# Performance work log

Measured on AMD Instinct MI355X. Metric: run time of the kernel, lower is better.

Reference implementation:

```python
import jax, jax.numpy as jnp
import numpy as np

EPS = 1e-8
UNTANH = 0.5                       # hp UNTANH (blend factor, assumed)
BUNTANH_SCALE = (2.0 + 2.0 ** 0.5) ** 0.5  # sqrt(2 + sqrt(2)) from source
C_MOMENT = 0.99                    # hp c_moment
A_VARIANCE = 0.02                  # hp a_variance
SINKHORN_ITERS = 8


def rms_norm(x, axes):
    ms = jnp.mean(x * x, axis=axes, keepdims=True)
    return x * jax.lax.rsqrt(ms + EPS)


def buntanh(x):
    # blended un-tanh: untanh * identity + (1-untanh) * tanh, rescaled
    return BUNTANH_SCALE * (UNTANH * x + (1.0 - UNTANH) * jnp.tanh(x))


def sinkhorn_knopp(A, n_iter=SINKHORN_ITERS):
    A = jnp.maximum(A, 0.0) + EPS
    def body(A, _):
        A = A / jnp.sum(A, axis=-1, keepdims=True)  # row normalize
        A = A / jnp.sum(A, axis=-2, keepdims=True)  # col normalize
        return A, None
    A, _ = jax.lax.scan(body, A, None, length=n_iter)
    return A


def setup_inputs() -> dict:
    key = jax.random.key(0)
    ks = jax.random.split(key, 8)
    B, N, D, IN_DIM = 4, 1024, 128, 8192
    inv_sqrt_d = 1.0 / np.sqrt(D)
    return {
        "state": jax.random.normal(ks[0], (B, N, D), jnp.float32) * 0.1,
        "output": jax.random.normal(ks[1], (B, N, D), jnp.float32) * 0.1,
        "w1": jax.random.normal(ks[2], (B, N, D, D), jnp.float32) * inv_sqrt_d,
        "w2": jax.random.normal(ks[3], (B, N, D, D), jnp.float32) * inv_sqrt_d,
        "w3": jax.random.normal(ks[4], (B, N, D, D), jnp.float32) * inv_sqrt_d,
        "A_ema": jax.random.normal(ks[5], (B, N, N), jnp.float32) * 0.01,
        "env_input": jax.random.normal(ks[6], (B, IN_DIM), jnp.float32),
        "noise": jax.random.normal(ks[7], (B, N, D), jnp.float32),
    }


def reference(state, output, w1, w2, w3, A_ema, env_input, noise):
    B, N, D = state.shape
    input_dim = env_input.shape[1]
    num_in = -(-input_dim // D)  # ceil

    # first-call mask/EMA adjustment (num_input_nodes change branch)
    A_mask = jnp.ones((N, N), dtype=state.dtype).at[:num_in, :].set(0.0)
    A_ema = A_ema.at[:, num_in, :num_in].add(3.0 / num_in)

    # per-node batched small GEMMs + custom activation
    Q = buntanh(jnp.einsum('bnd,bndk->bnk', state, w3))
    K = buntanh(jnp.einsum('bnd,bndk->bnk', state, w2))
    prediction = buntanh(jnp.einsum('bnd,bndk->bnk', state, w1))

    # QK^T adjacency, rms-normed over full [N,N]
    raw_A = jnp.einsum('bnk,bmk->bnm', Q, K) / jnp.sqrt(jnp.asarray(D, state.dtype))
    raw_A = rms_norm(raw_A, (-2, -1))

    # EMA (non-first step) + input-node masking
    new_A_ema = (A_ema * C_MOMENT + raw_A * (1.0 - C_MOMENT)) * A_mask

    # doubly-stochastic projection, thresholded sparsification, re-project
    dsA = sinkhorn_knopp(new_A_ema)
    baseline = 1.0 / (N + 1.0)
    sparse_A = jnp.where(dsA > baseline, dsA, 0.0)
    A = sinkhorn_knopp(sparse_A) * A_mask

    # boredom noise scaled by variance deficit (torch var is unbiased)
    var = jnp.var(A, axis=(-2, -1), keepdims=True, ddof=1)
    vd = jax.nn.relu(A_VARIANCE - var)
    V = output + vd * noise

    # message passing + softsign, overwrite input-node rows with env input
    target = jax.nn.soft_sign(jnp.einsum('bnm,bmd->bnd', A, V))
    pad = num_in * D - input_dim
    env = jnp.pad(env_input, ((0, 0), (0, pad))).reshape(B, num_in, D)
    target = target.at[:, :num_in, :].set(env)

    out = jnp.concatenate([target, prediction], axis=-1)  # [B,N,2D]
    return out, A
```

## Files before the change

kernel.cpp:

```cpp
#include <hip/hip_runtime.h>
#include <math.h>

#define NB 4
#define NN 1024
#define ND 128
#define NUM_IN 64
#define F_EPS 1e-8f
#define BT_SCALE 1.8477590650225735f
#define INV_SQRT_D 0.08838834764831844f
#define BASELINE (1.0f/1025.0f)
#define OUT_STRIDE 256
#define A_OFF 1048576

__device__ __forceinline__ float buntanh_f(float x) {
    return BT_SCALE * (0.5f * x + 0.5f * tanhf(x));
}
__device__ __forceinline__ float wave_sum(float v) {
    #pragma unroll
    for (int off = 32; off > 0; off >>= 1) v += __shfl_xor(v, off, 64);
    return v;
}
__device__ __forceinline__ float bflo(unsigned u) { return __uint_as_float(u << 16); }
__device__ __forceinline__ float bfhi(unsigned u) { return __uint_as_float(u & 0xffff0000u); }
__device__ __forceinline__ unsigned bf_rne(float f) {
    unsigned x = __float_as_uint(f);
    return (x + 0x7fffu + ((x >> 16) & 1u)) >> 16;
}
__device__ __forceinline__ unsigned bf_pack(float lo, float hi) {
    return bf_rne(lo) | (bf_rne(hi) << 16);
}

typedef float f32x4 __attribute__((ext_vector_type(4)));
__device__ __forceinline__ float4 ntload4(const float4* p) {
    f32x4 v = __builtin_nontemporal_load((const f32x4*)p);
    return make_float4(v.x, v.y, v.z, v.w);
}

__global__ __launch_bounds__(256, 6) void qkp_kernel(
    const float* __restrict__ state,
    const float* __restrict__ w1,
    const float* __restrict__ w2,
    const float* __restrict__ w3,
    float* __restrict__ dout,
    float* __restrict__ Qg,
    float* __restrict__ Kg)
{
    const int blk = blockIdx.x;
    const int node = ((blk & 7) << 9) | (blk >> 3);

    __shared__ float s_state[ND];
    __shared__ float4 red[3][8][32];

    const int t = threadIdx.x;
    if (t < 32) ((float4*)s_state)[t] =
        ((const float4*)(state + ((size_t)node << 7)))[t];
    __syncthreads();

    const int g = t >> 5, m = t & 31;

    auto do_mat = [&](const float* wbase, int q) {
        const float4* w4 = (const float4*)(wbase + ((size_t)node << 14));
        float4 wv[8];
        float4 acc = make_float4(0.f, 0.f, 0.f, 0.f);
        #pragma unroll
        for (int i = 0; i < 8; ++i) wv[i] = ntload4(&w4[i*256 + t]);
        #pragma unroll
        for (int i = 0; i < 8; ++i) {
            const float s = s_state[i*8 + g];
            acc.x += s*wv[i].x; acc.y += s*wv[i].y;
            acc.z += s*wv[i].z; acc.w += s*wv[i].w;
        }
        #pragma unroll
        for (int i = 0; i < 8; ++i) wv[i] = ntload4(&w4[(8+i)*256 + t]);
        #pragma unroll
        for (int i = 0; i < 8; ++i) {
            const float s = s_state[(8+i)*8 + g];
            acc.x += s*wv[i].x; acc.y += s*wv[i].y;
            acc.z += s*wv[i].z; acc.w += s*wv[i].w;
        }
        red[q][g][m] = acc;
    };
    do_mat(w1, 0);
    do_mat(w2, 1);
    do_mat(w3, 2);
    __syncthreads();

    if (t < 96) {
        const int q = t >> 5, mm = t & 31;
        float4 o = red[q][0][mm];
        #pragma unroll
        for (int gg = 1; gg < 8; ++gg) {
            const float4 r = red[q][gg][mm];
            o.x += r.x; o.y += r.y; o.z += r.z; o.w += r.w;
        }
        o.x = buntanh_f(o.x); o.y = buntanh_f(o.y);
        o.z = buntanh_f(o.z); o.w = buntanh_f(o.w);
        if (q == 0) {
            *(float4*)(dout + (size_t)node * OUT_STRIDE + ND + 4*mm) = o;
        } else {
            float* base = (q == 1) ? Kg : Qg;
            *(float4*)(base + ((size_t)node << 7) + 4*mm) = o;
        }
    }
}

__global__ __launch_bounds__(256) void qk2_kernel(
    const float* __restrict__ Qg, const float* __restrict__ Kg,
    unsigned* __restrict__ rawbf, float* __restrict__ reds)
{
    const int b = blockIdx.x >> 10;
    const int tile = blockIdx.x & 1023;
    const int tr = tile >> 5, tc = tile & 31;

    __shared__ float Qs[32][132];
    __shared__ float Ks[32][136];
    __shared__ float wr4[4];

    const int t = threadIdx.x;
    for (int i = t; i < 1024; i += 256) {
        const int r = i >> 5, q = i & 31;
        *(float4*)&Qs[r][q*4] = *(const float4*)(Qg + (((size_t)(b*NN + tr*32 + r)) << 7) + q*4);
        *(float4*)&Ks[r][q*4] = *(const float4*)(Kg + (((size_t)(b*NN + tc*32 + r)) << 7) + q*4);
    }
    __syncthreads();

    const int ty = t >> 4;
    const int tx = t & 15;
    float a00=0.f, a01=0.f, a10=0.f, a11=0.f;
    #pragma unroll
    for (int dq = 0; dq < 32; ++dq) {
        const float4 q0 = *(const float4*)&Qs[ty][dq*4];
        const float4 q1 = *(const float4*)&Qs[ty+16][dq*4];
        const float4 k0 = *(const float4*)&Ks[2*tx][dq*4];
        const float4 k1 = *(const float4*)&Ks[2*tx+1][dq*4];
        a00 += q0.x*k0.x + q0.y*k0.y + q0.z*k0.z + q0.w*k0.w;
        a01 += q0.x*k1.x + q0.y*k1.y + q0.z*k1.z + q0.w*k1.w;
        a10 += q1.x*k0.x + q1.y*k0.y + q1.z*k0.z + q1.w*k0.w;
        a11 += q1.x*k1.x + q1.y*k1.y + q1.z*k1.z + q1.w*k1.w;
    }
    a00 *= INV_SQRT_D; a01 *= INV_SQRT_D; a10 *= INV_SQRT_D; a11 *= INV_SQRT_D;

    unsigned* r0p = rawbf + (((size_t)(b*NN + tr*32 + ty)) << 9) + tc*16;
    unsigned* r1p = rawbf + (((size_t)(b*NN + tr*32 + ty + 16)) << 9) + tc*16;
    r0p[tx] = bf_pack(a00, a01);
    r1p[tx] = bf_pack(a10, a11);

    float ssq = a00*a00 + a01*a01 + a10*a10 + a11*a11;
    ssq = wave_sum(ssq);
    if ((t & 63) == 0) wr4[t >> 6] = ssq;
    __syncthreads();
    if (t == 0) atomicAdd(&reds[b], wr4[0]+wr4[1]+wr4[2]+wr4[3]);
}

__global__ __launch_bounds__(256) void emaT_kernel(
    const unsigned* __restrict__ rawbf, const float* __restrict__ A_ema,
    const float* __restrict__ reds,
    unsigned* __restrict__ M0, unsigned* __restrict__ M0T,
    float* __restrict__ SR)
{
    const int b = blockIdx.x >> 8;
    const int tile = blockIdx.x & 255;
    const int tr = tile >> 4, tc = tile & 15;
    const int R0 = tr << 6, C0 = tc << 6;

    __shared__ float st[64][65];
    __shared__ float s_part[64][5];

    const int t = threadIdx.x;
    const int r = t >> 2, q = t & 3;
    const int row = R0 + r;
    const float scale = rsqrtf(reds[b] * (1.0f/1048576.0f) + F_EPS);

    const unsigned* rawrow = rawbf + (((size_t)(b*NN + row)) << 9) + tc*8*4;
    const uint4 u0 = ((const uint4*)rawrow)[q*2];
    const uint4 u1 = ((const uint4*)rawrow)[q*2 + 1];
    float rv[16];
    rv[0]=bflo(u0.x); rv[1]=bfhi(u0.x); rv[2]=bflo(u0.y); rv[3]=bfhi(u0.y);
    rv[4]=bflo(u0.z); rv[5]=bfhi(u0.z); rv[6]=bflo(u0.w); rv[7]=bfhi(u0.w);
    rv[8]=bflo(u1.x); rv[9]=bfhi(u1.x); rv[10]=bflo(u1.y); rv[11]=bfhi(u1.y);
    rv[12]=bflo(u1.z); rv[13]=bfhi(u1.z); rv[14]=bflo(u1.w); rv[15]=bfhi(u1.w);

    const float* emarow = A_ema + (((size_t)(b*NN + row)) << 10) + C0 + q*16;
    float s = 0.f;
    #pragma unroll
    for (int j = 0; j < 4; ++j) {
        const float4 e = ((const float4*)emarow)[j];
        float ev[4] = {e.x, e.y, e.z, e.w};
        #pragma unroll
        for (int k = 0; k < 4; ++k) {
            const int e_idx = j*4 + k;
            const int c = C0 + q*16 + e_idx;
            float em = ev[k];
            if (row == NUM_IN && c < NUM_IN) em += 3.0f / NUM_IN;
            float v = em * 0.99f + rv[e_idx] * scale * 0.01f;
            if (row < NUM_IN) v = 0.f;
            v = fmaxf(v, 0.f) + F_EPS;
            rv[e_idx] = v;
            st[r][q*16 + e_idx] = v;
            s += v;
        }
    }
    s_part[r][q] = s;

    unsigned* m0row = M0 + (((size_t)(b*NN + row)) << 9) + tc*8*4;
    uint4 o0, o1;
    o0.x = bf_pack(rv[0],rv[1]);  o0.y = bf_pack(rv[2],rv[3]);
    o0.z = bf_pack(rv[4],rv[5]);  o0.w = bf_pack(rv[6],rv[7]);
    o1.x = bf_pack(rv[8],rv[9]);  o1.y = bf_pack(rv[10],rv[11]);
    o1.z = bf_pack(rv[12],rv[13]); o1.w = bf_pack(rv[14],rv[15]);
    ((uint4*)m0row)[q*2]     = o0;
    ((uint4*)m0row)[q*2 + 1] = o1;
    __syncthreads();

    if (t < 64) {
        const float rs = s_part[t][0] + s_part[t][1] + s_part[t][2] + s_part[t][3];
        atomicAdd(&SR[b*NN + R0 + t], rs);
    }

    const int cT = t >> 2;
    float tv[16];
    #pragma unroll
    for (int k = 0; k < 16; ++k) tv[k] = st[q*16 + k][cT];
    uint4 w0, w1;
    w0.x = bf_pack(tv[0],tv[1]);  w0.y = bf_pack(tv[2],tv[3]);
    w0.z = bf_pack(tv[4],tv[5]);  w0.w = bf_pack(tv[6],tv[7]);
    w1.x = bf_pack(tv[8],tv[9]);  w1.y = bf_pack(tv[10],tv[11]);
    w1.z = bf_pack(tv[12],tv[13]); w1.w = bf_pack(tv[14],tv[15]);
    unsigned* mtrow = M0T + (((size_t)(b*NN + C0 + cT)) << 9) + tr*8*4;
    ((uint4*)mtrow)[q*2]     = w0;
    ((uint4*)mtrow)[q*2 + 1] = w1;
}

template<bool INV_IN>
__global__ __launch_bounds__(256) void mv_kernel(
    const unsigned* __restrict__ Abf, const float* __restrict__ x,
    float* __restrict__ y)
{
    const int blk = blockIdx.x;
    const int lp  = ((blk & 7) << 5) | (blk >> 3);
    const int b   = lp >> 6;
    const int r0  = (lp & 63) << 4;
    const int t = threadIdx.x;
    const int w = t >> 6, l = t & 63;

    const float4* xb = (const float4*)(x + (b << 10));
    float4 x0 = xb[2*l], x1 = xb[2*l+1], x2 = xb[128+2*l], x3 = xb[129+2*l];
    if (INV_IN) {
        x0.x=1.f/x0.x; x0.y=1.f/x0.y; x0.z=1.f/x0.z; x0.w=1.f/x0.w;
        x1.x=1.f/x1.x; x1.y=1.f/x1.y; x1.z=1.f/x1.z; x1.w=1.f/x1.w;
        x2.x=1.f/x2.x; x2.y=1.f/x2.y; x2.z=1.f/x2.z; x2.w=1.f/x2.w;
        x3.x=1.f/x3.x; x3.y=1.f/x3.y; x3.z=1.f/x3.z; x3.w=1.f/x3.w;
    }

    #pragma unroll
    for (int r = 0; r < 4; ++r) {
        const int row = r0 + (w << 2) + r;
        const unsigned* rp = Abf + (((size_t)((b << 10) + row)) << 9);
        const uint4 v0 = ((const uint4*)rp)[l];
        const uint4 v1 = ((const uint4*)rp)[64 + l];
        float a = bflo(v0.x)*x0.x + bfhi(v0.x)*x0.y
                + bflo(v0.y)*x0.z + bfhi(v0.y)*x0.w
                + bflo(v0.z)*x1.x + bfhi(v0.z)*x1.y
                + bflo(v0.w)*x1.z + bfhi(v0.w)*x1.w
                + bflo(v1.x)*x2.x + bfhi(v1.x)*x2.y
                + bflo(v1.y)*x2.z + bfhi(v1.y)*x2.w
                + bflo(v1.z)*x3.x + bfhi(v1.z)*x3.y
                + bflo(v1.w)*x3.z + bfhi(v1.w)*x3.w;
        a = wave_sum(a);
        if (l == 0) y[(b << 10) + row] = 1.0f / a;
    }
}

__global__ __launch_bounds__(256) void thresh_kernel(
    const unsigned* __restrict__ M0, const unsigned* __restrict__ M0T,
    const float* __restrict__ r8, const float* __restrict__ c8,
    unsigned* __restrict__ A1, unsigned* __restrict__ A1T,
    float* __restrict__ SR2)
{
    const int t = threadIdx.x;
    const int b = blockIdx.x >> 6;
    const int g0 = (blockIdx.x & 63) << 4;
    const int w = t >> 6, l = t & 63;
    const bool doA1 = (w < 2);
    const int wr = doA1 ? w : (w - 2);
    const unsigned* src = doA1 ? M0 : M0T;
    unsigned*       dst = doA1 ? A1 : A1T;
    const float* rowS = doA1 ? r8 : c8;
    const float* colS = doA1 ? c8 : r8;

    const float4* cb = (const float4*)(colS + (b << 10));
    const float4 c0 = cb[2*l], c1 = cb[2*l+1], c2 = cb[128+2*l], c3 = cb[129+2*l];
    const float cm[16] = {c0.x,c0.y,c0.z,c0.w, c1.x,c1.y,c1.z,c1.w,
                          c2.x,c2.y,c2.z,c2.w, c3.x,c3.y,c3.z,c3.w};

    for (int rr = 0; rr < 8; ++rr) {
        const int row = g0 + wr*8 + rr;
        const float ri = rowS[(b << 10) + row];
        const unsigned* rp = src + (((size_t)(b*NN + row)) << 9);
        const uint4 v0 = ((const uint4*)rp)[l];
        const uint4 v1 = ((const uint4*)rp)[64 + l];
        float e[16];
        e[0]=bflo(v0.x); e[1]=bfhi(v0.x); e[2]=bflo(v0.y); e[3]=bfhi(v0.y);
        e[4]=bflo(v0.z); e[5]=bfhi(v0.z); e[6]=bflo(v0.w); e[7]=bfhi(v0.w);
        e[8]=bflo(v1.x); e[9]=bfhi(v1.x); e[10]=bflo(v1.y); e[11]=bfhi(v1.y);
        e[12]=bflo(v1.z); e[13]=bfhi(v1.z); e[14]=bflo(v1.w); e[15]=bfhi(v1.w);
        float s = 0.f;
        #pragma unroll
        for (int j = 0; j < 16; ++j) {
            const float d = e[j] * ri * cm[j];
            e[j] = (d > BASELINE ? d : 0.f) + F_EPS;
            s += e[j];
        }
        uint4 o0, o1;
        o0.x = bf_pack(e[0],e[1]);  o0.y = bf_pack(e[2],e[3]);
        o0.z = bf_pack(e[4],e[5]);  o0.w = bf_pack(e[6],e[7]);
        o1.x = bf_pack(e[8],e[9]);  o1.y = bf_pack(e[10],e[11]);
        o1.z = bf_pack(e[12],e[13]); o1.w = bf_pack(e[14],e[15]);
        unsigned* op = dst + (((size_t)(b*NN + row)) << 9);
        ((uint4*)op)[l] = o0;
        ((uint4*)op)[64 + l] = o1;
        if (doA1) {
            s = wave_sum(s);
            if (l == 0) SR2[b*NN + row] = s;
        }
    }
}

__global__ __launch_bounds__(256) void fin_kernel(
    const unsigned* __restrict__ A1, const float* __restrict__ r8,
    const float* __restrict__ c8, float* __restrict__ reds,
    float* __restrict__ dout)
{
    __shared__ float wred[8];
    const int t = threadIdx.x;
    const int b = blockIdx.x >> 6;
    const int g0 = (blockIdx.x & 63) << 4;
    const int w = t >> 6, l = t & 63;

    const float4* cb = (const float4*)(c8 + (b << 10));
    const float4 c0 = cb[2*l], c1 = cb[2*l+1], c2 = cb[128+2*l], c3 = cb[129+2*l];
    const float cm[16] = {c0.x,c0.y,c0.z,c0.w, c1.x,c1.y,c1.z,c1.w,
                          c2.x,c2.y,c2.z,c2.w, c3.x,c3.y,c3.z,c3.w};

    float s1 = 0.f, s2 = 0.f;
    for (int rr = 0; rr < 4; ++rr) {
        const int row = g0 + w*4 + rr;
        float* Arow = dout + A_OFF + (((size_t)(b*NN + row)) << 10);
        if (row < NUM_IN) {
            const float4 z = make_float4(0.f,0.f,0.f,0.f);
            ((float4*)Arow)[2*l] = z;       ((float4*)Arow)[2*l+1] = z;
            ((float4*)Arow)[128+2*l] = z;   ((float4*)Arow)[129+2*l] = z;
        } else {
            const float ri = r8[(b << 10) + row];
            const unsigned* rp = A1 + (((size_t)(b*NN + row)) << 9);
            const uint4 v0 = ((const uint4*)rp)[l];
            const uint4 v1 = ((const uint4*)rp)[64 + l];
            float e[16];
            e[0]=bflo(v0.x); e[1]=bfhi(v0.x); e[2]=bflo(v0.y); e[3]=bfhi(v0.y);
            e[4]=bflo(v0.z); e[5]=bfhi(v0.z); e[6]=bflo(v0.w); e[7]=bfhi(v0.w);
            e[8]=bflo(v1.x); e[9]=bfhi(v1.x); e[10]=bflo(v1.y); e[11]=bfhi(v1.y);
            e[12]=bflo(v1.z); e[13]=bfhi(v1.z); e[14]=bflo(v1.w); e[15]=bfhi(v1.w);
            #pragma unroll
            for (int j = 0; j < 16; ++j) {
                e[j] = e[j] * ri * cm[j];
                s1 += e[j]; s2 += e[j]*e[j];
            }
            ((float4*)Arow)[2*l]     = make_float4(e[0],e[1],e[2],e[3]);
            ((float4*)Arow)[2*l+1]   = make_float4(e[4],e[5],e[6],e[7]);
            ((float4*)Arow)[128+2*l] = make_float4(e[8],e[9],e[10],e[11]);
            ((float4*)Arow)[129+2*l] = make_float4(e[12],e[13],e[14],e[15]);
        }
    }
    s1 = wave_sum(s1); s2 = wave_sum(s2);
    if (l == 0) { wred[w] = s1; wred[4 + w] = s2; }
    __syncthreads();
    if (t == 0) {
        atomicAdd(&reds[4 + b], wred[0]+wred[1]+wred[2]+wred[3]);
        atomicAdd(&reds[8 + b], wred[4]+wred[5]+wred[6]+wred[7]);
    }
}

__global__ __launch_bounds__(256) void vbuild_kernel(
    const float* __restrict__ outp, const float* __restrict__ noise,
    const float* __restrict__ reds, float* __restrict__ V)
{
    const int i = blockIdx.x * 256 + threadIdx.x;
    const int b = i >> 15;
    const float Mn = 1048576.f;
    const float S1 = reds[4 + b], S2 = reds[8 + b];
    const float var = (S2 - S1*S1/Mn) / (Mn - 1.f);
    const float vd = fmaxf(0.02f - var, 0.f);
    const float4 o = ((const float4*)outp)[i];
    const float4 n = ((const float4*)noise)[i];
    ((float4*)V)[i] = make_float4(o.x + vd*n.x, o.y + vd*n.y,
                                  o.z + vd*n.z, o.w + vd*n.w);
}

__global__ __launch_bounds__(256) void av_part(
    const float* __restrict__ A,
    const float* __restrict__ V,
    float* __restrict__ P)
{
    const int bid = blockIdx.x;
    const int ks = bid & 3;
    const int rt = (bid >> 2) % 60;
    const int b  = bid / 240;
    const int r0 = NUM_IN + rt * 16;
    const int mc0 = ks << 8;
    const int t = threadIdx.x;
    const int d = t & 127, rg = t >> 7;
    const int rowb = r0 + rg*8;

    float acc[8] = {0.f,0.f,0.f,0.f,0.f,0.f,0.f,0.f};
    const float* Vb = V + ((size_t)b << 17) + ((size_t)mc0 << 7) + d;
    const float* Ab = A + (((size_t)(b*NN + rowb)) << 10) + mc0;

    #pragma unroll 4
    for (int mq = 0; mq < 64; ++mq) {
        const float v0 = Vb[(mq*4 + 0) << 7];
        const float v1 = Vb[(mq*4 + 1) << 7];
        const float v2 = Vb[(mq*4 + 2) << 7];
        const float v3 = Vb[(mq*4 + 3) << 7];
        #pragma unroll
        for (int k = 0; k < 8; ++k) {
            const float4 a = *(const float4*)(Ab + ((size_t)k << 10) + mq*4);
            acc[k] += a.x*v0 + a.y*v1 + a.z*v2 + a.w*v3;
        }
    }
    #pragma unroll
    for (int k = 0; k < 8; ++k) {
        const int ridx = rt*16 + rg*8 + k;
        P[(((size_t)(ks*NB + b)) * 960 + ridx) * 128 + d] = acc[k];
    }
}

__global__ __launch_bounds__(256) void av_fin(
    const float* __restrict__ P, const float* __restrict__ env,
    float* __restrict__ dout)
{
    const int t = threadIdx.x;
    int bid = blockIdx.x;
    if (bid < 128) {
        const int idx = bid*256 + t;
        const int b = idx >> 13, off = idx & 8191;
        const int r = off >> 7, d = off & 127;
        dout[((size_t)(b*NN + r)) * OUT_STRIDE + d] = env[idx];
        return;
    }
    bid -= 128;
    const int idx = bid*256 + t;
    const int d = idx & 127;
    const int rd = idx >> 7;
    const int b = rd / 960;
    const int ridx = rd - b*960;
    const float s = P[idx] + P[idx + 491520] + P[idx + 2*491520] + P[idx + 3*491520];
    dout[((size_t)(b*NN + NUM_IN + ridx)) * OUT_STRIDE + d] = s / (1.f + fabsf(s));
}

extern "C" void kernel_launch(void* const* d_in, const int* in_sizes, int n_in,
                              void* d_out, int out_size, void* d_ws, size_t ws_size,
                              hipStream_t stream)
{
    (void)in_sizes; (void)n_in; (void)out_size; (void)ws_size;
    const float* state = (const float*)d_in[0];
    const float* outp  = (const float*)d_in[1];
    const float* w1    = (const float*)d_in[2];
    const float* w2    = (const float*)d_in[3];
    const float* w3    = (const float*)d_in[4];
    const float* A_ema = (const float*)d_in[5];
    const float* env   = (const float*)d_in[6];
    const float* noise = (const float*)d_in[7];
    float* dout = (float*)d_out;

    unsigned* M0  = (unsigned*)(dout + A_OFF);
    unsigned* M0T = M0 + 2097152;

    float*    Qg   = (float*)d_ws;
    float*    Kg   = Qg + 524288;
    float*    Vg   = Kg + 524288;
    unsigned* raw  = (unsigned*)(Vg + 524288);
    unsigned* A1   = raw;
    unsigned* A1T  = raw + 2097152;
    float*    Pp   = (float*)A1T;
    float*    SR1  = (float*)(A1T + 2097152);
    float*    reds = SR1 + 4096;
    float*    SC1  = reds + 16;
    float*    SR2  = SC1 + 4096;
    float*    SC2  = SR2 + 4096;
    float*    RV1  = SC2 + 4096;
    float*    RV2  = RV1 + 4096;

    hipMemsetAsync(SR1, 0, (4096 + 16) * sizeof(float), stream);

    qkp_kernel<<<dim3(NB*NN), dim3(256), 0, stream>>>(
        state, w1, w2, w3, dout, Qg, Kg);

    qk2_kernel<<<dim3(NB*1024), dim3(256), 0, stream>>>(Qg, Kg, raw, reds);

    emaT_kernel<<<dim3(NB*256), dim3(256), 0, stream>>>(
        raw, A_ema, reds, M0, M0T, SR1);

    mv_kernel<true ><<<dim3(256), dim3(256), 0, stream>>>(M0T, SR1, SC1);
    for (int k = 1; k < 15; ++k) {
        if (k & 1)
            mv_kernel<false><<<dim3(256), dim3(256), 0, stream>>>(M0, SC1, RV1);
        else
            mv_kernel<false><<<dim3(256), dim3(256), 0, stream>>>(M0T, RV1, SC1);
    }

    thresh_kernel<<<dim3(NB*64), dim3(256), 0, stream>>>(
        M0, M0T, RV1, SC1, A1, A1T, SR2);

    mv_kernel<true ><<<dim3(256), dim3(256), 0, stream>>>(A1T, SR2, SC2);
    for (int k = 1; k < 15; ++k) {
        if (k & 1)
            mv_kernel<false><<<dim3(256), dim3(256), 0, stream>>>(A1, SC2, RV2);
        else
            mv_kernel<false><<<dim3(256), dim3(256), 0, stream>>>(A1T, RV2, SC2);
    }

    fin_kernel<<<dim3(NB*64), dim3(256), 0, stream>>>(A1, RV2, SC2, reds, dout);

    vbuild_kernel<<<dim3(512), dim3(256), 0, stream>>>(outp, noise, reds, Vg);

    av_part<<<dim3(960), dim3(256), 0, stream>>>(dout + A_OFF, Vg, Pp);

    av_fin<<<dim3(2048), dim3(256), 0, stream>>>(Pp, env, dout);
}
```

Baseline: 422.1 us.

## Split prediction GEMV out of QK kernel and spread it across later kernels

The w1 prediction GEMV is removed from the fused per-node Q/K/P kernel. It is distributed as extra tail blocks appended to the grids of later kernels: qk2, emaT, every Sinkhorn mat-vec, thresh, fin and av_part. The latency-bound, under-occupied kernels such as the 256-block mat-vecs then carry useful bandwidth work, and the first kernel reads one third less weight data. In exchange, each host kernel gains extra blocks and a branch. The prediction work now competes for bandwidth with the critical-path stages.

```diff
diff --git a/kernel.cpp b/kernel.cpp
--- a/kernel.cpp
+++ b/kernel.cpp
@@ -36,12 +36,47 @@
     return make_float4(v.x, v.y, v.z, v.w);
 }
 
-__global__ __launch_bounds__(256, 6) void qkp_kernel(
+__device__ __forceinline__ void pred_node(
+    const int node, const float* __restrict__ state,
+    const float* __restrict__ w1, float* __restrict__ dout)
+{
+    __shared__ float4 pred_red[8][32];
+    const int t = threadIdx.x;
+    const int g = t >> 5, m = t & 31;
+    const float4* w4 = (const float4*)(w1 + ((size_t)node << 14));
+    const float* srow = state + ((size_t)node << 7);
+    float4 acc = make_float4(0.f, 0.f, 0.f, 0.f);
+    #pragma unroll
+    for (int h = 0; h < 2; ++h) {
+        float4 wv[8];
+        #pragma unroll
+        for (int i = 0; i < 8; ++i) wv[i] = ntload4(&w4[(h*8 + i)*256 + t]);
+        #pragma unroll
+        for (int i = 0; i < 8; ++i) {
+            const float s = srow[(h*8 + i)*8 + g];
+            acc.x += s*wv[i].x; acc.y += s*wv[i].y;
+            acc.z += s*wv[i].z; acc.w += s*wv[i].w;
+        }
+    }
+    pred_red[g][m] = acc;
+    __syncthreads();
+    if (t < 32) {
+        float4 o = pred_red[0][t];
+        #pragma unroll
+        for (int gg = 1; gg < 8; ++gg) {
+            const float4 r = pred_red[gg][t];
+            o.x += r.x; o.y += r.y; o.z += r.z; o.w += r.w;
+        }
+        o.x = buntanh_f(o.x); o.y = buntanh_f(o.y);
+        o.z = buntanh_f(o.z); o.w = buntanh_f(o.w);
+        *(float4*)(dout + (size_t)node * OUT_STRIDE + ND + 4*t) = o;
+    }
+}
+
+__global__ __launch_bounds__(256, 8) void qk_kernel(
     const float* __restrict__ state,
-    const float* __restrict__ w1,
     const float* __restrict__ w2,
     const float* __restrict__ w3,
-    float* __restrict__ dout,
     float* __restrict__ Qg,
     float* __restrict__ Kg)
 {
@@ -49,7 +84,7 @@
     const int node = ((blk & 7) << 9) | (blk >> 3);
 
     __shared__ float s_state[ND];
-    __shared__ float4 red[3][8][32];
+    __shared__ float4 red[2][8][32];
 
     const int t = threadIdx.x;
     if (t < 32) ((float4*)s_state)[t] =
@@ -80,12 +115,11 @@
         }
         red[q][g][m] = acc;
     };
-    do_mat(w1, 0);
-    do_mat(w2, 1);
-    do_mat(w3, 2);
+    do_mat(w2, 0);
+    do_mat(w3, 1);
     __syncthreads();
 
-    if (t < 96) {
+    if (t < 64) {
         const int q = t >> 5, mm = t & 31;
         float4 o = red[q][0][mm];
         #pragma unroll
@@ -95,19 +129,21 @@
         }
         o.x = buntanh_f(o.x); o.y = buntanh_f(o.y);
         o.z = buntanh_f(o.z); o.w = buntanh_f(o.w);
-        if (q == 0) {
-            *(float4*)(dout + (size_t)node * OUT_STRIDE + ND + 4*mm) = o;
-        } else {
-            float* base = (q == 1) ? Kg : Qg;
-            *(float4*)(base + ((size_t)node << 7) + 4*mm) = o;
-        }
+        float* base = (q == 0) ? Kg : Qg;
+        *(float4*)(base + ((size_t)node << 7) + 4*mm) = o;
     }
 }
 
 __global__ __launch_bounds__(256) void qk2_kernel(
     const float* __restrict__ Qg, const float* __restrict__ Kg,
-    unsigned* __restrict__ rawbf, float* __restrict__ reds)
-{
+    unsigned* __restrict__ rawbf, float* __restrict__ reds,
+    const float* __restrict__ state, const float* __restrict__ w1,
+    float* __restrict__ dout, int predBase)
+{
+    if (blockIdx.x >= 4096) {
+        pred_node(predBase + (int)blockIdx.x - 4096, state, w1, dout);
+        return;
+    }
     const int b = blockIdx.x >> 10;
     const int tile = blockIdx.x & 1023;
     const int tr = tile >> 5, tc = tile & 31;
@@ -156,8 +192,14 @@
     const unsigned* __restrict__ rawbf, const float* __restrict__ A_ema,
     const float* __restrict__ reds,
     unsigned* __restrict__ M0, unsigned* __restrict__ M0T,
-    float* __restrict__ SR)
-{
+    float* __restrict__ SR,
+    const float* __restrict__ state, const float* __restrict__ w1,
+    float* __restrict__ dout, int predBase)
+{
+    if (blockIdx.x >= 1024) {
+        pred_node(predBase + (int)blockIdx.x - 1024, state, w1, dout);
+        return;
+    }
     const int b = blockIdx.x >> 8;
     const int tile = blockIdx.x & 255;
     const int tr = tile >> 4, tc = tile & 15;
@@ -221,22 +263,28 @@
     float tv[16];
     #pragma unroll
     for (int k = 0; k < 16; ++k) tv[k] = st[q*16 + k][cT];
-    uint4 w0, w1;
+    uint4 w0, w1v;
     w0.x = bf_pack(tv[0],tv[1]);  w0.y = bf_pack(tv[2],tv[3]);
     w0.z = bf_pack(tv[4],tv[5]);  w0.w = bf_pack(tv[6],tv[7]);
-    w1.x = bf_pack(tv[8],tv[9]);  w1.y = bf_pack(tv[10],tv[11]);
-    w1.z = bf_pack(tv[12],tv[13]); w1.w = bf_pack(tv[14],tv[15]);
+    w1v.x = bf_pack(tv[8],tv[9]);  w1v.y = bf_pack(tv[10],tv[11]);
+    w1v.z = bf_pack(tv[12],tv[13]); w1v.w = bf_pack(tv[14],tv[15]);
     unsigned* mtrow = M0T + (((size_t)(b*NN + C0 + cT)) << 9) + tr*8*4;
     ((uint4*)mtrow)[q*2]     = w0;
-    ((uint4*)mtrow)[q*2 + 1] = w1;
+    ((uint4*)mtrow)[q*2 + 1] = w1v;
 }
 
 template<bool INV_IN>
 __global__ __launch_bounds__(256) void mv_kernel(
     const unsigned* __restrict__ Abf, const float* __restrict__ x,
-    float* __restrict__ y)
+    float* __restrict__ y,
+    const float* __restrict__ state, const float* __restrict__ w1,
+    float* __restrict__ dout, int predBase)
 {
     const int blk = blockIdx.x;
+    if (blk >= 256) {
+        pred_node(predBase + blk - 256, state, w1, dout);
+        return;
+    }
     const int lp  = ((blk & 7) << 5) | (blk >> 3);
     const int b   = lp >> 6;
     const int r0  = (lp & 63) << 4;
@@ -275,8 +323,14 @@
     const unsigned* __restrict__ M0, const unsigned* __restrict__ M0T,
     const float* __restrict__ r8, const float* __restrict__ c8,
     unsigned* __restrict__ A1, unsigned* __restrict__ A1T,
-    float* __restrict__ SR2)
-{
+    float* __restrict__ SR2,
+    const float* __restrict__ state, const float* __restrict__ w1,
+    float* __restrict__ dout, int predBase)
+{
+    if (blockIdx.x >= 256) {
+        pred_node(predBase + (int)blockIdx.x - 256, state, w1, dout);
+        return;
+    }
     const int t = threadIdx.x;
     const int b = blockIdx.x >> 6;
     const int g0 = (blockIdx.x & 63) << 4;
@@ -329,8 +383,14 @@
 __global__ __launch_bounds__(256) void fin_kernel(
     const unsigned* __restrict__ A1, const float* __restrict__ r8,
     const float* __restrict__ c8, float* __restrict__ reds,
-    float* __restrict__ dout)
-{
+    float* __restrict__ dout,
+    const float* __restrict__ state, const float* __restrict__ w1,
+    int predBase)
+{
+    if (blockIdx.x >= 256) {
+        pred_node(predBase + (int)blockIdx.x - 256, state, w1, dout);
+        return;
+    }
     __shared__ float wred[8];
     const int t = threadIdx.x;
     const int b = blockIdx.x >> 6;
@@ -397,10 +457,15 @@
 }
 
 __global__ __launch_bounds__(256) void av_part(
-    const float* __restrict__ A,
-    const float* __restrict__ V,
-    float* __restrict__ P)
-{
+    const float* __restrict__ A, const float* __restrict__ V,
+    float* __restrict__ P,
+    const float* __restrict__ state, const float* __restrict__ w1,
+    float* __restrict__ dout, int predBase)
+{
+    if (blockIdx.x >= 960) {
+        pred_node(predBase + (int)blockIdx.x - 960, state, w1, dout);
+        return;
+    }
     const int bid = blockIdx.x;
     const int ks = bid & 3;
     const int rt = (bid >> 2) % 60;
@@ -492,38 +557,56 @@
 
     hipMemsetAsync(SR1, 0, (4096 + 16) * sizeof(float), stream);
 
-    qkp_kernel<<<dim3(NB*NN), dim3(256), 0, stream>>>(
-        state, w1, w2, w3, dout, Qg, Kg);
-
-    qk2_kernel<<<dim3(NB*1024), dim3(256), 0, stream>>>(Qg, Kg, raw, reds);
-
-    emaT_kernel<<<dim3(NB*256), dim3(256), 0, stream>>>(
-        raw, A_ema, reds, M0, M0T, SR1);
-
-    mv_kernel<true ><<<dim3(256), dim3(256), 0, stream>>>(M0T, SR1, SC1);
+    qk_kernel<<<dim3(NB*NN), dim3(256), 0, stream>>>(state, w2, w3, Qg, Kg);
+
+    int pb = 0;
+    qk2_kernel<<<dim3(4096 + 512), dim3(256), 0, stream>>>(
+        Qg, Kg, raw, reds, state, w1, dout, pb);
+    pb += 512;
+
+    emaT_kernel<<<dim3(1024 + 512), dim3(256), 0, stream>>>(
+        raw, A_ema, reds, M0, M0T, SR1, state, w1, dout, pb);
+    pb += 512;
+
+    mv_kernel<true ><<<dim3(256 + 64), dim3(256), 0, stream>>>(
+        M0T, SR1, SC1, state, w1, dout, pb);
+    pb += 64;
     for (int k = 1; k < 15; ++k) {
         if (k & 1)
-            mv_kernel<false><<<dim3(256), dim3(256), 0, stream>>>(M0, SC1, RV1);
+            mv_kernel<false><<<dim3(256 + 64), dim3(256), 0, stream>>>(
+                M0, SC1, RV1, state, w1, dout, pb);
         else
-            mv_kernel<false><<<dim3(256), dim3(256), 0, stream>>>(M0T, RV1, SC1);
-    }
-
-    thresh_kernel<<<dim3(NB*64), dim3(256), 0, stream>>>(
-        M0, M0T, RV1, SC1, A1, A1T, SR2);
-
-    mv_kernel<true ><<<dim3(256), dim3(256), 0, stream>>>(A1T, SR2, SC2);
+            mv_kernel<false><<<dim3(256 + 64), dim3(256), 0, stream>>>(
+                M0T, RV1, SC1, state, w1, dout, pb);
+        pb += 64;
+    }
+
+    thresh_kernel<<<dim3(256 + 384), dim3(256), 0, stream>>>(
+        M0, M0T, RV1, SC1, A1, A1T, SR2, state, w1, dout, pb);
+    pb += 384;
+
+    mv_kernel<true ><<<dim3(256 + 64), dim3(256), 0, stream>>>(
+        A1T, SR2, SC2, state, w1, dout, pb);
+    pb += 64;
     for (int k = 1; k < 15; ++k) {
         if (k & 1)
-            mv_kernel<false><<<dim3(256), dim3(256), 0, stream>>>(A1, SC2, RV2);
+            mv_kernel<false><<<dim3(256 + 64), dim3(256), 0, stream>>>(
+                A1, SC2, RV2, state, w1, dout, pb);
         else
-            mv_kernel<false><<<dim3(256), dim3(256), 0, stream>>>(A1T, RV2, SC2);
-    }
-
-    fin_kernel<<<dim3(NB*64), dim3(256), 0, stream>>>(A1, RV2, SC2, reds, dout);
+            mv_kernel<false><<<dim3(256 + 64), dim3(256), 0, stream>>>(
+                A1T, RV2, SC2, state, w1, dout, pb);
+        pb += 64;
+    }
+
+    fin_kernel<<<dim3(256 + 384), dim3(256), 0, stream>>>(
+        A1, RV2, SC2, reds, dout, state, w1, pb);
+    pb += 384;
 
     vbuild_kernel<<<dim3(512), dim3(256), 0, stream>>>(outp, noise, reds, Vg);
 
-    av_part<<<dim3(960), dim3(256), 0, stream>>>(dout + A_OFF, Vg, Pp);
+    av_part<<<dim3(960 + 384), dim3(256), 0, stream>>>(
+        dout + A_OFF, Vg, Pp, state, w1, dout, pb);
+    pb += 384;
 
     av_fin<<<dim3(2048), dim3(256), 0, stream>>>(Pp, env, dout);
 }
```

New measurement: 437.4 us (median of 2 runs). +3.6%, slower.
